# Performance work log

Hardware: AMD Instinct MI355X
Metric: run time of the kernel (lower is better)

Reference implementation:

```python
import jax, jax.numpy as jnp
import numpy as np

N_NODES = 20000
IN_FEAT = 128
CONV_OUT = 32
N_EDGES = 640000
FC1_OUT = 128


def setup_inputs() -> dict:
    key = jax.random.key(0)
    ks = jax.random.split(key, 8)
    x = jax.random.normal(ks[0], (N_NODES, IN_FEAT), dtype=jnp.float32)
    edge_index = jax.random.randint(ks[1], (2, N_EDGES), 0, N_NODES, dtype=jnp.int64)
    # GCNConv params (PyG: lin weight [in, out] applied as x @ W, plus bias)
    w_conv = jax.random.normal(ks[2], (IN_FEAT, CONV_OUT), dtype=jnp.float32) * (1.0 / np.sqrt(IN_FEAT))
    b_conv = jnp.zeros((CONV_OUT,), dtype=jnp.float32)
    # fc1: Linear(32*N -> 128), torch stores weight as [out, in]
    w_fc1 = jax.random.normal(ks[3], (FC1_OUT, CONV_OUT * N_NODES), dtype=jnp.float32) * (1.0 / np.sqrt(CONV_OUT * N_NODES))
    b_fc1 = jnp.zeros((FC1_OUT,), dtype=jnp.float32)
    # fc2: Linear(128 -> N)
    w_fc2 = jax.random.normal(ks[4], (N_NODES, FC1_OUT), dtype=jnp.float32) * (1.0 / np.sqrt(FC1_OUT))
    b_fc2 = jnp.zeros((N_NODES,), dtype=jnp.float32)
    return {"x": x, "edge_index": edge_index, "w_conv": w_conv, "b_conv": b_conv,
            "w_fc1": w_fc1, "b_fc1": b_fc1, "w_fc2": w_fc2, "b_fc2": b_fc2}


def gcn_conv(x, edge_index, w, b):
    # PyG GCNConv default: add self-loops, symmetric normalization D^-1/2 (A+I) D^-1/2
    n = x.shape[0]
    loop = jnp.arange(n, dtype=edge_index.dtype)
    src = jnp.concatenate([edge_index[0], loop])  # [E+N]
    dst = jnp.concatenate([edge_index[1], loop])
    deg = jax.ops.segment_sum(jnp.ones_like(dst, dtype=x.dtype), dst, num_segments=n)
    dinv = jnp.where(deg > 0, jax.lax.rsqrt(deg), 0.0)
    norm = dinv[src] * dinv[dst]  # [E+N]
    h = x @ w  # [N, out] — transform before propagate
    msg = h[src] * norm[:, None]  # gather
    agg = jax.ops.segment_sum(msg, dst, num_segments=n)  # scatter-add
    return agg + b


def reference(x, edge_index, w_conv, b_conv, w_fc1, b_fc1, w_fc2, b_fc2):
    h1 = jax.nn.relu(gcn_conv(x, edge_index, w_conv, b_conv))  # [N, 32]; dropout inactive (eval)
    flat = h1.reshape(-1, CONV_OUT * N_NODES)  # [1, 32*N]
    h3 = jax.nn.relu(flat @ w_fc1.T + b_fc1)   # [1, 128]
    out = jax.nn.relu(h3 @ w_fc2.T + b_fc2)    # [1, N] q-values
    return out
```

## Files before the change

kernel.cpp:

```cpp
#include <hip/hip_runtime.h>

#define N_NODES 20000
#define IN_FEAT 128
#define CONV_OUT 32
#define N_EDGES 640000
#define FC1_OUT 128


#define ZERO_WORDS 20000

__global__ __launch_bounds__(256) void k_zero(float4* __restrict__ p) {
    int i = blockIdx.x * 256 + threadIdx.x;
    if (i < ZERO_WORDS / 4) p[i] = make_float4(0.f, 0.f, 0.f, 0.f);
}

__global__ __launch_bounds__(256) void k_degslot(const int* __restrict__ ei,
                                                 int* __restrict__ cnt,
                                                 int* __restrict__ r) {
    int t = blockIdx.x * 256 + threadIdx.x;
    if (t < N_EDGES / 4) {
        int4 d = ((const int4*)(ei + N_EDGES))[t];
        int4 s;
        s.x = atomicAdd(&cnt[d.x], 1);
        s.y = atomicAdd(&cnt[d.y], 1);
        s.z = atomicAdd(&cnt[d.z], 1);
        s.w = atomicAdd(&cnt[d.w], 1);
        ((int4*)r)[t] = s;
    }
}

#define SCAN_T 1024
#define SCAN_CHUNK 20
__global__ __launch_bounds__(1024) void k_scan(const int* __restrict__ cnt,
                                               int* __restrict__ startv,
                                               float* __restrict__ dinv) {
    __shared__ int ld[SCAN_T * SCAN_CHUNK];
    __shared__ int ps[SCAN_T];
    int t = threadIdx.x;
    const int4* c4 = (const int4*)cnt;
    int4* l4 = (int4*)ld;
    #pragma unroll
    for (int i = 0; i < 5; ++i) {
        int idx = i * SCAN_T + t;
        l4[idx] = (idx < N_NODES / 4) ? c4[idx] : make_int4(0, 0, 0, 0);
    }
    __syncthreads();
    int local[SCAN_CHUNK];
    int base = t * SCAN_CHUNK;
    int sum = 0;
    #pragma unroll
    for (int i = 0; i < SCAN_CHUNK; ++i) { local[i] = ld[base + i]; sum += local[i]; }
    ps[t] = sum;
    __syncthreads();
    for (int off = 1; off < SCAN_T; off <<= 1) {
        int v = (t >= off) ? ps[t - off] : 0;
        __syncthreads();
        ps[t] += v;
        __syncthreads();
    }
    int run = (t == 0) ? 0 : ps[t - 1];
    #pragma unroll
    for (int i = 0; i < SCAN_CHUNK; ++i) {
        int n = base + i;
        ld[n] = run;
        if (n < N_NODES) dinv[n] = rsqrtf((float)local[i] + 1.0f);
        run += local[i];
    }
    __syncthreads();
    const int4* l4c = (const int4*)ld;
    int4* s4 = (int4*)startv;
    #pragma unroll
    for (int i = 0; i < 5; ++i) {
        int idx = i * SCAN_T + t;
        if (idx < N_NODES / 4) s4[idx] = l4c[idx];
    }
    if (t == 0) startv[N_NODES] = N_EDGES;
}

__global__ __launch_bounds__(256) void k_gemm1(const float* __restrict__ x,
                                               const float* __restrict__ w,
                                               const float* __restrict__ dinv,
                                               float* __restrict__ h) {
    __shared__ float xs[64][132];
    __shared__ float ws[128][32];
    int tid = threadIdx.x;
    int n0 = blockIdx.x * 64;

    const float4* w4 = (const float4*)w;
    float4* ws4 = (float4*)ws;
    #pragma unroll
    for (int i = 0; i < 4; ++i) ws4[i * 256 + tid] = w4[i * 256 + tid];

    const float4* x4 = (const float4*)x;
    #pragma unroll
    for (int i = 0; i < 8; ++i) {
        int idx = i * 256 + tid;
        int nl  = idx >> 5;
        int k4  = idx & 31;
        int n   = n0 + nl;
        float4 v = make_float4(0.f, 0.f, 0.f, 0.f);
        if (n < N_NODES) v = x4[(size_t)n * 32 + k4];
        *(float4*)&xs[nl][k4 * 4] = v;
    }
    __syncthreads();

    int c4  = tid & 7;
    int nl0 = tid >> 3;
    const float4* wsrow = (const float4*)ws;
    #pragma unroll
    for (int p = 0; p < 2; ++p) {
        int nl = nl0 + p * 32;
        float4 acc = make_float4(0.f, 0.f, 0.f, 0.f);
        #pragma unroll 8
        for (int k = 0; k < 128; k += 4) {
            float4 xv  = *(const float4*)&xs[nl][k];
            float4 wv0 = wsrow[(k + 0) * 8 + c4];
            float4 wv1 = wsrow[(k + 1) * 8 + c4];
            float4 wv2 = wsrow[(k + 2) * 8 + c4];
            float4 wv3 = wsrow[(k + 3) * 8 + c4];
            acc.x += xv.x * wv0.x + xv.y * wv1.x + xv.z * wv2.x + xv.w * wv3.x;
            acc.y += xv.x * wv0.y + xv.y * wv1.y + xv.z * wv2.y + xv.w * wv3.y;
            acc.z += xv.x * wv0.z + xv.y * wv1.z + xv.z * wv2.z + xv.w * wv3.z;
            acc.w += xv.x * wv0.w + xv.y * wv1.w + xv.z * wv2.w + xv.w * wv3.w;
        }
        int n = n0 + nl;
        if (n < N_NODES) {
            float dv = dinv[n];
            acc.x *= dv; acc.y *= dv; acc.z *= dv; acc.w *= dv;
            *(float4*)&h[(size_t)n * 32 + c4 * 4] = acc;
        }
    }
}

__global__ __launch_bounds__(256) void k_fill(const int* __restrict__ ei,
                                              const int* __restrict__ startv,
                                              const int* __restrict__ r,
                                              int* __restrict__ csr) {
    int e = blockIdx.x * 256 + threadIdx.x;
    if (e < N_EDGES) {
        int s = ei[e];
        int d = ei[N_EDGES + e];
        csr[startv[d] + r[e]] = s;
    }
}

__global__ __launch_bounds__(256) void k_gather(const int* __restrict__ startv,
                                                const int* __restrict__ csr,
                                                const float* __restrict__ h,
                                                const float* __restrict__ dinv,
                                                const float* __restrict__ bc,
                                                float* __restrict__ flat) {
    int tid  = threadIdx.x;
    int lane = tid & 63;
    int n    = blockIdx.x * 4 + (tid >> 6);
    if (n >= N_NODES) return;
    int es = lane >> 3;
    int f4 = lane & 7;
    const float4* h4 = (const float4*)h;
    float4 acc = make_float4(0.f, 0.f, 0.f, 0.f);
    int p0 = startv[n], p1 = startv[n + 1];
    #pragma unroll 2
    for (int p = p0 + es; p < p1; p += 8) {
        int s = csr[p];
        float4 v = h4[(size_t)s * 8 + f4];
        acc.x += v.x; acc.y += v.y; acc.z += v.z; acc.w += v.w;
    }
    #pragma unroll
    for (int m = 8; m < 64; m <<= 1) {
        acc.x += __shfl_xor(acc.x, m);
        acc.y += __shfl_xor(acc.y, m);
        acc.z += __shfl_xor(acc.z, m);
        acc.w += __shfl_xor(acc.w, m);
    }
    if (lane < 8) {
        float4 self = h4[(size_t)n * 8 + f4];
        float dv = dinv[n];
        float4 b = ((const float4*)bc)[f4];
        float4 r_;
        r_.x = fmaxf((acc.x + self.x) * dv + b.x, 0.f);
        r_.y = fmaxf((acc.y + self.y) * dv + b.y, 0.f);
        r_.z = fmaxf((acc.z + self.z) * dv + b.z, 0.f);
        r_.w = fmaxf((acc.w + self.w) * dv + b.w, 0.f);
        ((float4*)flat)[(size_t)n * 8 + f4] = r_;
    }
}

#define FC1_CH 25
__global__ __launch_bounds__(256) void k_fc1(const float* __restrict__ flat,
                                             const float* __restrict__ w,
                                             float* __restrict__ part) {
    int bid = blockIdx.x;
    int jg = bid & 31;
    int ch = bid >> 5;
    int j0 = jg * 4;
    const float4* f4 = (const float4*)flat;
    const size_t row4 = (size_t)CONV_OUT * N_NODES / 4;
    const float4* w0 = (const float4*)w + (size_t)(j0 + 0) * row4;
    const float4* w1 = (const float4*)w + (size_t)(j0 + 1) * row4;
    const float4* w2 = (const float4*)w + (size_t)(j0 + 2) * row4;
    const float4* w3 = (const float4*)w + (size_t)(j0 + 3) * row4;
    int base = ch * 6400;
    float a0 = 0.f, a1 = 0.f, a2 = 0.f, a3 = 0.f;
    #pragma unroll 5
    for (int it = 0; it < 25; ++it) {
        int k = base + it * 256 + threadIdx.x;
        float4 fv  = f4[k];
        float4 v0  = w0[k];
        float4 v1  = w1[k];
        float4 v2  = w2[k];
        float4 v3  = w3[k];
        a0 += v0.x * fv.x + v0.y * fv.y + v0.z * fv.z + v0.w * fv.w;
        a1 += v1.x * fv.x + v1.y * fv.y + v1.z * fv.z + v1.w * fv.w;
        a2 += v2.x * fv.x + v2.y * fv.y + v2.z * fv.z + v2.w * fv.w;
        a3 += v3.x * fv.x + v3.y * fv.y + v3.z * fv.z + v3.w * fv.w;
    }
    #pragma unroll
    for (int o = 32; o > 0; o >>= 1) {
        a0 += __shfl_down(a0, o);
        a1 += __shfl_down(a1, o);
        a2 += __shfl_down(a2, o);
        a3 += __shfl_down(a3, o);
    }
    __shared__ float red[4][4];
    int wv = threadIdx.x >> 6;
    if ((threadIdx.x & 63) == 0) {
        red[wv][0] = a0; red[wv][1] = a1; red[wv][2] = a2; red[wv][3] = a3;
    }
    __syncthreads();
    if (threadIdx.x < 4) {
        float s = red[0][threadIdx.x] + red[1][threadIdx.x] +
                  red[2][threadIdx.x] + red[3][threadIdx.x];
        part[(size_t)(j0 + threadIdx.x) * FC1_CH + ch] = s;
    }
}

__global__ __launch_bounds__(256) void k_fc2(const float* __restrict__ part,
                                             const float* __restrict__ b1,
                                             const float* __restrict__ w2,
                                             const float* __restrict__ b2,
                                             float* __restrict__ out) {
    __shared__ float h3s[128];
    int tid = threadIdx.x;
    if (tid < 128) {
        const float* p = part + (size_t)tid * FC1_CH;
        float s = 0.f;
        #pragma unroll
        for (int i = 0; i < FC1_CH; ++i) s += p[i];
        h3s[tid] = fmaxf(s + b1[tid], 0.f);
    }
    __syncthreads();
    int i = blockIdx.x * 256 + tid;
    if (i < N_NODES) {
        const float4* wr = (const float4*)(w2 + (size_t)i * FC1_OUT);
        const float4* h4 = (const float4*)h3s;
        float acc = b2[i];
        #pragma unroll
        for (int j = 0; j < 32; ++j) {
            float4 wv = wr[j];
            float4 hv = h4[j];
            acc += wv.x * hv.x + wv.y * hv.y + wv.z * hv.z + wv.w * hv.w;
        }
        out[i] = fmaxf(acc, 0.f);
    }
}

extern "C" void kernel_launch(void* const* d_in, const int* in_sizes, int n_in,
                              void* d_out, int out_size, void* d_ws, size_t ws_size,
                              hipStream_t stream) {
    const float* x      = (const float*)d_in[0];
    const int*   ei     = (const int*)d_in[1];
    const float* w_conv = (const float*)d_in[2];
    const float* b_conv = (const float*)d_in[3];
    const float* w_fc1  = (const float*)d_in[4];
    const float* b_fc1  = (const float*)d_in[5];
    const float* w_fc2  = (const float*)d_in[6];
    const float* b_fc2  = (const float*)d_in[7];
    float* ws = (float*)d_ws;
    int*   cnt    = (int*)ws;
    float* part   = ws + 20000;
    int*   startv = (int*)(ws + 23200);
    float* dinv   = ws + 43204;
    int*   r      = (int*)(ws + 63204);
    int*   csr    = (int*)(ws + 703204);
    float* h      = ws + 1343204;
    float* flat   = ws + 1983204;
    float* out    = (float*)d_out;

    k_zero<<<(ZERO_WORDS / 4 + 255) / 256, 256, 0, stream>>>((float4*)d_ws);
    k_degslot<<<(N_EDGES / 4 + 255) / 256, 256, 0, stream>>>(ei, cnt, r);
    k_scan<<<1, SCAN_T, 0, stream>>>(cnt, startv, dinv);
    k_gemm1<<<(N_NODES + 63) / 64, 256, 0, stream>>>(x, w_conv, dinv, h);
    k_fill<<<(N_EDGES + 255) / 256, 256, 0, stream>>>(ei, startv, r, csr);
    k_gather<<<(N_NODES + 3) / 4, 256, 0, stream>>>(startv, csr, h, dinv, b_conv, flat);
    k_fc1<<<32 * FC1_CH, 256, 0, stream>>>(flat, w_fc1, part);
    k_fc2<<<(N_NODES + 255) / 256, 256, 0, stream>>>(part, b_fc1, w_fc2, b_fc2, out);
}
```

Measured before the change: 165.2 us.

## Fuse zeroing into GEMM, merge degree count with last-block scan

Zeroing the count buffer and done ticket now happens in extra blocks of the GEMM kernel. Degree counting and the prefix scan share one kernel, where the last block to finish (found with an atomic ticket) runs the scan. The source-side dinv scaling moves out of the GEMM into the gather loop so the GEMM no longer depends on dinv, which cuts two kernel launches. In exchange the gather does an extra dinv load per edge, and the scan runs on a single 256-thread block with more serial work per thread.

```diff
diff --git a/kernel.cpp b/kernel.cpp
--- a/kernel.cpp
+++ b/kernel.cpp
@@ -7,83 +7,22 @@
 #define FC1_OUT 128
 
 
-#define ZERO_WORDS 20000
-
-__global__ __launch_bounds__(256) void k_zero(float4* __restrict__ p) {
-    int i = blockIdx.x * 256 + threadIdx.x;
-    if (i < ZERO_WORDS / 4) p[i] = make_float4(0.f, 0.f, 0.f, 0.f);
-}
-
-__global__ __launch_bounds__(256) void k_degslot(const int* __restrict__ ei,
-                                                 int* __restrict__ cnt,
-                                                 int* __restrict__ r) {
-    int t = blockIdx.x * 256 + threadIdx.x;
-    if (t < N_EDGES / 4) {
-        int4 d = ((const int4*)(ei + N_EDGES))[t];
-        int4 s;
-        s.x = atomicAdd(&cnt[d.x], 1);
-        s.y = atomicAdd(&cnt[d.y], 1);
-        s.z = atomicAdd(&cnt[d.z], 1);
-        s.w = atomicAdd(&cnt[d.w], 1);
-        ((int4*)r)[t] = s;
-    }
-}
-
-#define SCAN_T 1024
-#define SCAN_CHUNK 20
-__global__ __launch_bounds__(1024) void k_scan(const int* __restrict__ cnt,
-                                               int* __restrict__ startv,
-                                               float* __restrict__ dinv) {
-    __shared__ int ld[SCAN_T * SCAN_CHUNK];
-    __shared__ int ps[SCAN_T];
-    int t = threadIdx.x;
-    const int4* c4 = (const int4*)cnt;
-    int4* l4 = (int4*)ld;
-    #pragma unroll
-    for (int i = 0; i < 5; ++i) {
-        int idx = i * SCAN_T + t;
-        l4[idx] = (idx < N_NODES / 4) ? c4[idx] : make_int4(0, 0, 0, 0);
-    }
-    __syncthreads();
-    int local[SCAN_CHUNK];
-    int base = t * SCAN_CHUNK;
-    int sum = 0;
-    #pragma unroll
-    for (int i = 0; i < SCAN_CHUNK; ++i) { local[i] = ld[base + i]; sum += local[i]; }
-    ps[t] = sum;
-    __syncthreads();
-    for (int off = 1; off < SCAN_T; off <<= 1) {
-        int v = (t >= off) ? ps[t - off] : 0;
-        __syncthreads();
-        ps[t] += v;
-        __syncthreads();
-    }
-    int run = (t == 0) ? 0 : ps[t - 1];
-    #pragma unroll
-    for (int i = 0; i < SCAN_CHUNK; ++i) {
-        int n = base + i;
-        ld[n] = run;
-        if (n < N_NODES) dinv[n] = rsqrtf((float)local[i] + 1.0f);
-        run += local[i];
-    }
-    __syncthreads();
-    const int4* l4c = (const int4*)ld;
-    int4* s4 = (int4*)startv;
-    #pragma unroll
-    for (int i = 0; i < 5; ++i) {
-        int idx = i * SCAN_T + t;
-        if (idx < N_NODES / 4) s4[idx] = l4c[idx];
-    }
-    if (t == 0) startv[N_NODES] = N_EDGES;
-}
-
-__global__ __launch_bounds__(256) void k_gemm1(const float* __restrict__ x,
-                                               const float* __restrict__ w,
-                                               const float* __restrict__ dinv,
-                                               float* __restrict__ h) {
+#define GEMM1_BLOCKS 313
+#define ZERO_INT4 5001
+
+__global__ __launch_bounds__(256) void k1_gemm_zero(const float* __restrict__ x,
+                                                    const float* __restrict__ w,
+                                                    float* __restrict__ h,
+                                                    int4* __restrict__ zbase) {
     __shared__ float xs[64][132];
     __shared__ float ws[128][32];
     int tid = threadIdx.x;
+
+    if (blockIdx.x >= GEMM1_BLOCKS) {
+        int i = (blockIdx.x - GEMM1_BLOCKS) * 256 + tid;
+        if (i < ZERO_INT4) zbase[i] = make_int4(0, 0, 0, 0);
+        return;
+    }
     int n0 = blockIdx.x * 64;
 
     const float4* w4 = (const float4*)w;
@@ -124,12 +63,77 @@
             acc.w += xv.x * wv0.w + xv.y * wv1.w + xv.z * wv2.w + xv.w * wv3.w;
         }
         int n = n0 + nl;
-        if (n < N_NODES) {
-            float dv = dinv[n];
-            acc.x *= dv; acc.y *= dv; acc.z *= dv; acc.w *= dv;
-            *(float4*)&h[(size_t)n * 32 + c4 * 4] = acc;
-        }
-    }
+        if (n < N_NODES) *(float4*)&h[(size_t)n * 32 + c4 * 4] = acc;
+    }
+}
+
+__global__ __launch_bounds__(256) void k_degscan(const int* __restrict__ ei,
+                                                 int* __restrict__ cnt,
+                                                 int* __restrict__ r,
+                                                 int* __restrict__ done,
+                                                 int* __restrict__ startv,
+                                                 float* __restrict__ dinv) {
+    __shared__ int ld[20480];
+    __shared__ int ps[256];
+    __shared__ int sticket;
+    int tid = threadIdx.x;
+    int t = blockIdx.x * 256 + tid;
+
+    int4 d = ((const int4*)(ei + N_EDGES))[t];
+    int4 s;
+    s.x = atomicAdd(&cnt[d.x], 1);
+    s.y = atomicAdd(&cnt[d.y], 1);
+    s.z = atomicAdd(&cnt[d.z], 1);
+    s.w = atomicAdd(&cnt[d.w], 1);
+    ((int4*)r)[t] = s;
+
+    __syncthreads();
+    if (tid == 0) {
+        __threadfence();
+        sticket = atomicAdd(done, 1);
+    }
+    __syncthreads();
+    if (sticket != (int)gridDim.x - 1) return;
+
+    __threadfence();
+    const int4* c4 = (const int4*)cnt;
+    int4* l4 = (int4*)ld;
+    #pragma unroll
+    for (int i = 0; i < 20; ++i) {
+        int idx = i * 256 + tid;
+        l4[idx] = (idx < N_NODES / 4) ? c4[idx] : make_int4(0, 0, 0, 0);
+    }
+    __syncthreads();
+    int base = tid * 80;
+    int sum = 0;
+    #pragma unroll 8
+    for (int i = 0; i < 80; ++i) sum += ld[base + i];
+    ps[tid] = sum;
+    __syncthreads();
+    for (int off = 1; off < 256; off <<= 1) {
+        int v = (tid >= off) ? ps[tid - off] : 0;
+        __syncthreads();
+        ps[tid] += v;
+        __syncthreads();
+    }
+    int run = (tid == 0) ? 0 : ps[tid - 1];
+    #pragma unroll 8
+    for (int i = 0; i < 80; ++i) {
+        int n = base + i;
+        int v = ld[n];
+        ld[n] = run;
+        if (n < N_NODES) dinv[n] = rsqrtf((float)v + 1.0f);
+        run += v;
+    }
+    __syncthreads();
+    const int4* l4c = (const int4*)ld;
+    int4* s4 = (int4*)startv;
+    #pragma unroll
+    for (int i = 0; i < 20; ++i) {
+        int idx = i * 256 + tid;
+        if (idx < N_NODES / 4) s4[idx] = l4c[idx];
+    }
+    if (tid == 0) startv[N_NODES] = N_EDGES;
 }
 
 __global__ __launch_bounds__(256) void k_fill(const int* __restrict__ ei,
@@ -162,8 +166,9 @@
     #pragma unroll 2
     for (int p = p0 + es; p < p1; p += 8) {
         int s = csr[p];
+        float ds = dinv[s];
         float4 v = h4[(size_t)s * 8 + f4];
-        acc.x += v.x; acc.y += v.y; acc.z += v.z; acc.w += v.w;
+        acc.x += v.x * ds; acc.y += v.y * ds; acc.z += v.z * ds; acc.w += v.w * ds;
     }
     #pragma unroll
     for (int m = 8; m < 64; m <<= 1) {
@@ -173,14 +178,14 @@
         acc.w += __shfl_xor(acc.w, m);
     }
     if (lane < 8) {
+        float dv = dinv[n];
         float4 self = h4[(size_t)n * 8 + f4];
-        float dv = dinv[n];
         float4 b = ((const float4*)bc)[f4];
         float4 r_;
-        r_.x = fmaxf((acc.x + self.x) * dv + b.x, 0.f);
-        r_.y = fmaxf((acc.y + self.y) * dv + b.y, 0.f);
-        r_.z = fmaxf((acc.z + self.z) * dv + b.z, 0.f);
-        r_.w = fmaxf((acc.w + self.w) * dv + b.w, 0.f);
+        r_.x = fmaxf((acc.x + dv * self.x) * dv + b.x, 0.f);
+        r_.y = fmaxf((acc.y + dv * self.y) * dv + b.y, 0.f);
+        r_.z = fmaxf((acc.z + dv * self.z) * dv + b.z, 0.f);
+        r_.w = fmaxf((acc.w + dv * self.w) * dv + b.w, 0.f);
         ((float4*)flat)[(size_t)n * 8 + f4] = r_;
     }
 }
@@ -277,19 +282,18 @@
     const float* b_fc2  = (const float*)d_in[7];
     float* ws = (float*)d_ws;
     int*   cnt    = (int*)ws;
-    float* part   = ws + 20000;
-    int*   startv = (int*)(ws + 23200);
-    float* dinv   = ws + 43204;
-    int*   r      = (int*)(ws + 63204);
-    int*   csr    = (int*)(ws + 703204);
-    float* h      = ws + 1343204;
-    float* flat   = ws + 1983204;
+    int*   done   = (int*)(ws + 20000);
+    float* part   = ws + 20004;
+    int*   startv = (int*)(ws + 23204);
+    float* dinv   = ws + 43208;
+    int*   r      = (int*)(ws + 63208);
+    int*   csr    = (int*)(ws + 703208);
+    float* h      = ws + 1343208;
+    float* flat   = ws + 1983208;
     float* out    = (float*)d_out;
 
-    k_zero<<<(ZERO_WORDS / 4 + 255) / 256, 256, 0, stream>>>((float4*)d_ws);
-    k_degslot<<<(N_EDGES / 4 + 255) / 256, 256, 0, stream>>>(ei, cnt, r);
-    k_scan<<<1, SCAN_T, 0, stream>>>(cnt, startv, dinv);
-    k_gemm1<<<(N_NODES + 63) / 64, 256, 0, stream>>>(x, w_conv, dinv, h);
+    k1_gemm_zero<<<GEMM1_BLOCKS + 20, 256, 0, stream>>>(x, w_conv, h, (int4*)d_ws);
+    k_degscan<<<N_EDGES / 4 / 256, 256, 0, stream>>>(ei, cnt, r, done, startv, dinv);
     k_fill<<<(N_EDGES + 255) / 256, 256, 0, stream>>>(ei, startv, r, csr);
     k_gather<<<(N_NODES + 3) / 4, 256, 0, stream>>>(startv, csr, h, dinv, b_conv, flat);
     k_fc1<<<32 * FC1_CH, 256, 0, stream>>>(flat, w_fc1, part);
```

Result: slower. 177.4 us (+7.4%).
